# Performance work log

Measured on AMD Instinct MI355X. Metric: run time of the kernel, lower is better.

## Reference

```python
import jax, jax.numpy as jnp
import numpy as np

HIDDEN = 64
EPS = 1e-5  # torch LayerNorm default eps


def _layernorm(x, gamma, beta):
    mu = jnp.mean(x, axis=-1, keepdims=True)
    var = jnp.mean((x - mu) ** 2, axis=-1, keepdims=True)
    return (x - mu) * jax.lax.rsqrt(var + EPS) * gamma + beta


def setup_inputs() -> dict:
    key = jax.random.key(0)
    ks = jax.random.split(key, 9)
    N, E, H = 100000, 3200000, HIDDEN
    positions = jax.random.normal(ks[0], (N, 3), dtype=jnp.float32)
    velocities = jax.random.normal(ks[1], (N, 3), dtype=jnp.float32)
    edge_index = jax.random.randint(ks[2], (2, E), 0, N, dtype=jnp.int64)
    # Linear(8, H): torch init ~ U(-1/sqrt(8), 1/sqrt(8))
    b1_lim = 1.0 / np.sqrt(8.0)
    W1 = jax.random.uniform(ks[3], (8, H), jnp.float32, -b1_lim, b1_lim)
    b1 = jax.random.uniform(ks[4], (H,), jnp.float32, -b1_lim, b1_lim)
    b2_lim = 1.0 / np.sqrt(float(H))
    W2 = jax.random.uniform(ks[5], (H, H), jnp.float32, -b2_lim, b2_lim)
    b2 = jax.random.uniform(ks[6], (H,), jnp.float32, -b2_lim, b2_lim)
    g1 = jnp.ones((H,), jnp.float32)
    be1 = jnp.zeros((H,), jnp.float32)
    g2 = jnp.ones((H,), jnp.float32)
    be2 = jnp.zeros((H,), jnp.float32)
    return {"positions": positions, "velocities": velocities, "edge_index": edge_index,
            "W1": W1, "b1": b1, "g1": g1, "be1": be1,
            "W2": W2, "b2": b2, "g2": g2, "be2": be2}


def reference(positions, velocities, edge_index, W1, b1, g1, be1, W2, b2, g2, be2):
    src, tgt = edge_index[0], edge_index[1]
    r_ij = positions[tgt] - positions[src]                     # (E, 3)
    r_norm = jnp.linalg.norm(r_ij, axis=1, keepdims=True)      # (E, 1)
    v_rel = velocities[tgt] - velocities[src]                  # (E, 3)
    v_norm = jnp.linalg.norm(v_rel, axis=1, keepdims=True)     # (E, 1)
    feats = jnp.concatenate([r_ij, r_norm, v_rel, v_norm], axis=1)  # (E, 8)
    h = jax.nn.relu(_layernorm(feats @ W1 + b1, g1, be1))      # (E, H)
    h = jax.nn.relu(_layernorm(h @ W2 + b2, g2, be2))          # (E, H)
    return h
```

## Files before the change

### kernel.cpp

```cpp
#include <hip/hip_runtime.h>
#include <hip/hip_bf16.h>

#define H 64
#define EPS 1e-5f

__global__ void __launch_bounds__(256) edge_mlp_kernel(
    const float* __restrict__ pos,
    const float* __restrict__ vel,
    const int*   __restrict__ eidx,
    const float* __restrict__ W1,
    const float* __restrict__ b1,
    const float* __restrict__ g1,
    const float* __restrict__ be1,
    const float* __restrict__ W2,
    const float* __restrict__ b2,
    const float* __restrict__ g2,
    const float* __restrict__ be2,
    float* __restrict__ out,
    int E)
{
    const int e = blockIdx.x * 256 + threadIdx.x;
    if (e >= E) return;

    const int s = eidx[e];
    const int t = eidx[E + e];

    const float rx = pos[3*t+0] - pos[3*s+0];
    const float ry = pos[3*t+1] - pos[3*s+1];
    const float rz = pos[3*t+2] - pos[3*s+2];
    const float vx = vel[3*t+0] - vel[3*s+0];
    const float vy = vel[3*t+1] - vel[3*s+1];
    const float vz = vel[3*t+2] - vel[3*s+2];
    const float rn = sqrtf(rx*rx + ry*ry + rz*rz);
    const float vn = sqrtf(vx*vx + vy*vy + vz*vz);

    const float f[8] = {rx, ry, rz, rn, vx, vy, vz, vn};

    float h[H];
#pragma unroll
    for (int j = 0; j < H; ++j) {
        float a = b1[j];
#pragma unroll
        for (int k = 0; k < 8; ++k) a = fmaf(f[k], W1[k*H + j], a);
        h[j] = a;
    }

    {
        float m = 0.f;
#pragma unroll
        for (int j = 0; j < H; ++j) m += h[j];
        m *= (1.0f / H);
        float v = 0.f;
#pragma unroll
        for (int j = 0; j < H; ++j) { const float d = h[j] - m; v = fmaf(d, d, v); }
        v *= (1.0f / H);
        const float rs = rsqrtf(v + EPS);
#pragma unroll
        for (int j = 0; j < H; ++j) {
            const float y = fmaf((h[j] - m) * rs, g1[j], be1[j]);
            h[j] = fmaxf(y, 0.f);
        }
    }

    float acc[H];
#pragma unroll
    for (int j = 0; j < H; ++j) acc[j] = b2[j];
#pragma unroll
    for (int k = 0; k < H; ++k) {
        const float hk = h[k];
#pragma unroll
        for (int j = 0; j < H; ++j) acc[j] = fmaf(hk, W2[k*H + j], acc[j]);
    }

    {
        float m = 0.f;
#pragma unroll
        for (int j = 0; j < H; ++j) m += acc[j];
        m *= (1.0f / H);
        float v = 0.f;
#pragma unroll
        for (int j = 0; j < H; ++j) { const float d = acc[j] - m; v = fmaf(d, d, v); }
        v *= (1.0f / H);
        const float rs = rsqrtf(v + EPS);
#pragma unroll
        for (int j = 0; j < H; ++j) {
            const float y = fmaf((acc[j] - m) * rs, g2[j], be2[j]);
            acc[j] = fmaxf(y, 0.f);
        }
    }

    float* o = out + (size_t)e * H;
#pragma unroll
    for (int j = 0; j < H; j += 4) {
        float4 v4 = make_float4(acc[j], acc[j+1], acc[j+2], acc[j+3]);
        *reinterpret_cast<float4*>(o + j) = v4;
    }
}

extern "C" void kernel_launch(void* const* d_in, const int* in_sizes, int n_in,
                              void* d_out, int out_size, void* d_ws, size_t ws_size,
                              hipStream_t stream) {
    const float* pos = (const float*)d_in[0];
    const float* vel = (const float*)d_in[1];
    const int*  eidx = (const int*)d_in[2];
    const float* W1  = (const float*)d_in[3];
    const float* b1  = (const float*)d_in[4];
    const float* g1  = (const float*)d_in[5];
    const float* be1 = (const float*)d_in[6];
    const float* W2  = (const float*)d_in[7];
    const float* b2  = (const float*)d_in[8];
    const float* g2  = (const float*)d_in[9];
    const float* be2 = (const float*)d_in[10];
    float* out = (float*)d_out;

    const int E = in_sizes[2] / 2;
    const int grid = (E + 255) / 256;
    edge_mlp_kernel<<<grid, 256, 0, stream>>>(pos, vel, eidx, W1, b1, g1, be1,
                                              W2, b2, g2, be2, out, E);
}
```

Measured before the change: 1.404 ms.

## Rewrite edge MLP second layer with split-bf16 MFMA and wave-level tiling

Replaces the per-thread scalar 64x64 matmul with MFMA 16x16x32 bf16 instructions. Each fp32 value is split into hi/lo bf16 parts and three products are summed, to stay close to fp32 accuracy. The first layer and its LayerNorm statistics are computed per edge and staged in swizzled shared memory. The second LayerNorm is reduced with cross-lane shuffles, and each 64-thread block processes several 64-edge groups with W2 kept in registers. The aim is to cut the large ALU and register cost of the scalar matmul, at the price of some precision loss and stores that are no longer vectorized.

```diff
diff --git a/kernel.cpp b/kernel.cpp
--- a/kernel.cpp
+++ b/kernel.cpp
@@ -1,10 +1,24 @@
 #include <hip/hip_runtime.h>
-#include <hip/hip_bf16.h>
+
+typedef float v4f __attribute__((ext_vector_type(4)));
+typedef short bf8 __attribute__((ext_vector_type(8)));
 
 #define H 64
 #define EPS 1e-5f
-
-__global__ void __launch_bounds__(256) edge_mlp_kernel(
+#define GPB 8
+
+__device__ __forceinline__ unsigned short f2bf(float x) {
+    unsigned u = __float_as_uint(x);
+    unsigned r = (u + 0x7FFFu + ((u >> 16) & 1u)) >> 16;
+    return (unsigned short)r;
+}
+__device__ __forceinline__ float bf2f(unsigned short h) {
+    return __uint_as_float(((unsigned)h) << 16);
+}
+
+#define MFMA16(a, b, c) __builtin_amdgcn_mfma_f32_16x16x32_bf16((a), (b), (c), 0, 0, 0)
+
+__global__ void __launch_bounds__(64, 2) edge_mlp_mfma(
     const float* __restrict__ pos,
     const float* __restrict__ vel,
     const int*   __restrict__ eidx,
@@ -19,81 +33,176 @@
     float* __restrict__ out,
     int E)
 {
-    const int e = blockIdx.x * 256 + threadIdx.x;
-    if (e >= E) return;
-
-    const int s = eidx[e];
-    const int t = eidx[E + e];
-
-    const float rx = pos[3*t+0] - pos[3*s+0];
-    const float ry = pos[3*t+1] - pos[3*s+1];
-    const float rz = pos[3*t+2] - pos[3*s+2];
-    const float vx = vel[3*t+0] - vel[3*s+0];
-    const float vy = vel[3*t+1] - vel[3*s+1];
-    const float vz = vel[3*t+2] - vel[3*s+2];
-    const float rn = sqrtf(rx*rx + ry*ry + rz*rz);
-    const float vn = sqrtf(vx*vx + vy*vy + vz*vz);
-
-    const float f[8] = {rx, ry, rz, rn, vx, vy, vz, vn};
-
-    float h[H];
+    __shared__ v4f    hbuf[64 * 16];
+    __shared__ float2 scbuf[64];
+
+    const int L   = threadIdx.x;
+    const int g16 = L >> 4;
+    const int l16 = L & 15;
+
+    bf8 BH00, BL00, BH01, BL01, BH10, BL10, BH11, BL11,
+        BH20, BL20, BH21, BL21, BH30, BL30, BH31, BL31;
+#define LOAD_B(n, c, BH, BL) do {                                        \
+        const int col_ = (n)*16 + l16;                                   \
+        _Pragma("unroll")                                                \
+        for (int j = 0; j < 8; ++j) {                                    \
+            float w_ = W2[((c)*32 + g16*8 + j) * H + col_];              \
+            unsigned short hi_ = f2bf(w_);                               \
+            BH[j] = (short)hi_;                                          \
+            BL[j] = (short)f2bf(w_ - bf2f(hi_));                         \
+        }                                                                \
+    } while (0)
+    LOAD_B(0, 0, BH00, BL00); LOAD_B(0, 1, BH01, BL01);
+    LOAD_B(1, 0, BH10, BL10); LOAD_B(1, 1, BH11, BL11);
+    LOAD_B(2, 0, BH20, BL20); LOAD_B(2, 1, BH21, BL21);
+    LOAD_B(3, 0, BH30, BL30); LOAD_B(3, 1, BH31, BL31);
+#undef LOAD_B
+
+    v4f G10a, G10b, G11a, G11b, BE10a, BE10b, BE11a, BE11b;
 #pragma unroll
-    for (int j = 0; j < H; ++j) {
-        float a = b1[j];
+    for (int j = 0; j < 4; ++j) {
+        G10a[j]  = g1 [ 0 + g16*8 + j];
+        G10b[j]  = g1 [ 0 + g16*8 + 4 + j];
+        G11a[j]  = g1 [32 + g16*8 + j];
+        G11b[j]  = g1 [32 + g16*8 + 4 + j];
+        BE10a[j] = be1[ 0 + g16*8 + j];
+        BE10b[j] = be1[ 0 + g16*8 + 4 + j];
+        BE11a[j] = be1[32 + g16*8 + j];
+        BE11b[j] = be1[32 + g16*8 + 4 + j];
+    }
+    v4f B2f, G2f, BE2f;
 #pragma unroll
-        for (int k = 0; k < 8; ++k) a = fmaf(f[k], W1[k*H + j], a);
-        h[j] = a;
+    for (int n = 0; n < 4; ++n) {
+        B2f[n]  = b2 [n*16 + l16];
+        G2f[n]  = g2 [n*16 + l16];
+        BE2f[n] = be2[n*16 + l16];
     }
 
-    {
-        float m = 0.f;
+#define BUILD_A(c, Ga, Gb, Ba, Bb, AH, AL) do {                          \
+        const int q0_ = (c)*8 + g16*2;                                   \
+        v4f x0_ = hbuf[erow*16 + ((q0_)     ^ (erow & 7))];              \
+        v4f x1_ = hbuf[erow*16 + ((q0_ + 1) ^ (erow & 7))];              \
+        _Pragma("unroll")                                                \
+        for (int j = 0; j < 4; ++j) {                                    \
+            float y_ = fmaf(x0_[j], scv.x, scv.y);                       \
+            y_ = fmaxf(fmaf(y_, Ga[j], Ba[j]), 0.f);                     \
+            unsigned short h_ = f2bf(y_);                                \
+            AH[j] = (short)h_;                                           \
+            AL[j] = (short)f2bf(y_ - bf2f(h_));                         \
+            float z_ = fmaf(x1_[j], scv.x, scv.y);                       \
+            z_ = fmaxf(fmaf(z_, Gb[j], Bb[j]), 0.f);                     \
+            unsigned short h2_ = f2bf(z_);                               \
+            AH[j + 4] = (short)h2_;                                      \
+            AL[j + 4] = (short)f2bf(z_ - bf2f(h2_));                     \
+        }                                                                \
+    } while (0)
+
+#define ACC_N(acc, BHc0, BLc0, BHc1, BLc1) do {                          \
+        acc = MFMA16(AH0, BHc0, acc);                                    \
+        acc = MFMA16(AH0, BLc0, acc);                                    \
+        acc = MFMA16(AL0, BHc0, acc);                                    \
+        acc = MFMA16(AH1, BHc1, acc);                                    \
+        acc = MFMA16(AH1, BLc1, acc);                                    \
+        acc = MFMA16(AL1, BHc1, acc);                                    \
+    } while (0)
+
+#define STORE_N(n, acn) do {                                             \
+        _Pragma("unroll")                                                \
+        for (int r = 0; r < 4; ++r) {                                    \
+            float y_ = fmaf(fmaf(acn[r], RS2[r], C2[r]), G2f[n], BE2f[n]); \
+            y_ = fmaxf(y_, 0.f);                                         \
+            if (full || (ebase + r) < E)                                 \
+                out[(size_t)(ebase + r) * H + (n)*16 + l16] = y_;        \
+        }                                                                \
+    } while (0)
+
+#define M_TILE(m) do {                                                   \
+        const int erow = (m)*16 + l16;                                   \
+        const float2 scv = scbuf[erow];                                  \
+        bf8 AH0, AL0, AH1, AL1;                                          \
+        BUILD_A(0, G10a, G10b, BE10a, BE10b, AH0, AL0);                  \
+        BUILD_A(1, G11a, G11b, BE11a, BE11b, AH1, AL1);                  \
+        v4f ac0 = {0.f, 0.f, 0.f, 0.f};                                  \
+        v4f ac1 = ac0, ac2 = ac0, ac3 = ac0;                             \
+        ACC_N(ac0, BH00, BL00, BH01, BL01);                              \
+        ACC_N(ac1, BH10, BL10, BH11, BL11);                              \
+        ACC_N(ac2, BH20, BL20, BH21, BL21);                              \
+        ACC_N(ac3, BH30, BL30, BH31, BL31);                              \
+        ac0 += B2f[0]; ac1 += B2f[1]; ac2 += B2f[2]; ac3 += B2f[3];      \
+        v4f sv = ac0 + ac1 + ac2 + ac3;                                  \
+        v4f qv = ac0*ac0 + ac1*ac1 + ac2*ac2 + ac3*ac3;                  \
+        _Pragma("unroll")                                                \
+        for (int msk = 1; msk < 16; msk <<= 1) {                         \
+            sv[0] += __shfl_xor(sv[0], msk);                             \
+            sv[1] += __shfl_xor(sv[1], msk);                             \
+            sv[2] += __shfl_xor(sv[2], msk);                             \
+            sv[3] += __shfl_xor(sv[3], msk);                             \
+            qv[0] += __shfl_xor(qv[0], msk);                             \
+            qv[1] += __shfl_xor(qv[1], msk);                             \
+            qv[2] += __shfl_xor(qv[2], msk);                             \
+            qv[3] += __shfl_xor(qv[3], msk);                             \
+        }                                                                \
+        v4f RS2, C2;                                                     \
+        _Pragma("unroll")                                                \
+        for (int r = 0; r < 4; ++r) {                                    \
+            float mu_  = sv[r] * (1.0f / H);                             \
+            float var_ = fmaf(-mu_, mu_, qv[r] * (1.0f / H));            \
+            float rs_  = rsqrtf(var_ + EPS);                             \
+            RS2[r] = rs_;                                                \
+            C2[r]  = -mu_ * rs_;                                         \
+        }                                                                \
+        const int ebase = mb + (m)*16 + g16*4;                           \
+        STORE_N(0, ac0); STORE_N(1, ac1);                                \
+        STORE_N(2, ac2); STORE_N(3, ac3);                                \
+    } while (0)
+
+    int mb = blockIdx.x * (64 * GPB);
+    for (int it = 0; it < GPB; ++it, mb += 64) {
+        if (mb >= E) break;
+        const bool full = (mb + 64 <= E);
+
+        int e = mb + L;
+        if (e >= E) e = E - 1;
+        const int s = eidx[e];
+        const int t = eidx[E + e];
+        const float f0 = pos[3*t+0] - pos[3*s+0];
+        const float f1 = pos[3*t+1] - pos[3*s+1];
+        const float f2 = pos[3*t+2] - pos[3*s+2];
+        const float f3 = sqrtf(f0*f0 + f1*f1 + f2*f2);
+        const float f4 = vel[3*t+0] - vel[3*s+0];
+        const float f5 = vel[3*t+1] - vel[3*s+1];
+        const float f6 = vel[3*t+2] - vel[3*s+2];
+        const float f7 = sqrtf(f4*f4 + f5*f5 + f6*f6);
+
+        float m1 = 0.f, q1 = 0.f;
 #pragma unroll
-        for (int j = 0; j < H; ++j) m += h[j];
-        m *= (1.0f / H);
-        float v = 0.f;
-#pragma unroll
-        for (int j = 0; j < H; ++j) { const float d = h[j] - m; v = fmaf(d, d, v); }
-        v *= (1.0f / H);
-        const float rs = rsqrtf(v + EPS);
-#pragma unroll
-        for (int j = 0; j < H; ++j) {
-            const float y = fmaf((h[j] - m) * rs, g1[j], be1[j]);
-            h[j] = fmaxf(y, 0.f);
+        for (int q = 0; q < 16; ++q) {
+            v4f a = *(const v4f*)(b1 + 4*q);
+            a += f0 * *(const v4f*)(W1 + 0*H + 4*q);
+            a += f1 * *(const v4f*)(W1 + 1*H + 4*q);
+            a += f2 * *(const v4f*)(W1 + 2*H + 4*q);
+            a += f3 * *(const v4f*)(W1 + 3*H + 4*q);
+            a += f4 * *(const v4f*)(W1 + 4*H + 4*q);
+            a += f5 * *(const v4f*)(W1 + 5*H + 4*q);
+            a += f6 * *(const v4f*)(W1 + 6*H + 4*q);
+            a += f7 * *(const v4f*)(W1 + 7*H + 4*q);
+            m1 += a[0] + a[1] + a[2] + a[3];
+            q1 = fmaf(a[0], a[0], q1);
+            q1 = fmaf(a[1], a[1], q1);
+            q1 = fmaf(a[2], a[2], q1);
+            q1 = fmaf(a[3], a[3], q1);
+            hbuf[L*16 + (q ^ (L & 7))] = a;
         }
-    }
-
-    float acc[H];
-#pragma unroll
-    for (int j = 0; j < H; ++j) acc[j] = b2[j];
-#pragma unroll
-    for (int k = 0; k < H; ++k) {
-        const float hk = h[k];
-#pragma unroll
-        for (int j = 0; j < H; ++j) acc[j] = fmaf(hk, W2[k*H + j], acc[j]);
-    }
-
-    {
-        float m = 0.f;
-#pragma unroll
-        for (int j = 0; j < H; ++j) m += acc[j];
-        m *= (1.0f / H);
-        float v = 0.f;
-#pragma unroll
-        for (int j = 0; j < H; ++j) { const float d = acc[j] - m; v = fmaf(d, d, v); }
-        v *= (1.0f / H);
-        const float rs = rsqrtf(v + EPS);
-#pragma unroll
-        for (int j = 0; j < H; ++j) {
-            const float y = fmaf((acc[j] - m) * rs, g2[j], be2[j]);
-            acc[j] = fmaxf(y, 0.f);
-        }
-    }
-
-    float* o = out + (size_t)e * H;
-#pragma unroll
-    for (int j = 0; j < H; j += 4) {
-        float4 v4 = make_float4(acc[j], acc[j+1], acc[j+2], acc[j+3]);
-        *reinterpret_cast<float4*>(o + j) = v4;
+        const float mu1  = m1 * (1.0f / H);
+        const float var1 = fmaf(-mu1, mu1, q1 * (1.0f / H));
+        const float rs1  = rsqrtf(var1 + EPS);
+        scbuf[L] = make_float2(rs1, -mu1 * rs1);
+
+        __syncthreads();
+
+        M_TILE(0); M_TILE(1); M_TILE(2); M_TILE(3);
+
+        __syncthreads();
     }
 }
 
@@ -114,7 +223,7 @@
     float* out = (float*)d_out;
 
     const int E = in_sizes[2] / 2;
-    const int grid = (E + 255) / 256;
-    edge_mlp_kernel<<<grid, 256, 0, stream>>>(pos, vel, eidx, W1, b1, g1, be1,
-                                              W2, b2, g2, be2, out, E);
-}
+    const int grid = (E + 64 * GPB - 1) / (64 * GPB);
+    edge_mlp_mfma<<<grid, 64, 0, stream>>>(pos, vel, eidx, W1, b1, g1, be1,
+                                           W2, b2, g2, be2, out, E);
+}
```

Measured after the change: 1.124 ms. -19.9%, faster.
